# Optimization experiments

Measured on AMD Instinct MI355X. Metric: run time of the kernel, lower is better.

Reference implementation:

```python
import jax, jax.numpy as jnp
import numpy as np
import math

EPS = 1e-6
MAX_NORM = 1.0 - 1e-3


def _clip_to_ball(x):
    # Keep point strictly inside the unit ball (||x|| < 1).
    norm = jnp.maximum(jnp.linalg.norm(x, axis=-1, keepdims=True), EPS)
    factor = jnp.minimum(MAX_NORM / norm, 1.0)
    return x * factor


def setup_inputs() -> dict:
    key = jax.random.key(0)
    k1, k2 = jax.random.split(key)
    B, C, D = 8192, 4096, 512
    euclidean_emb = jax.random.normal(k1, (B, D), dtype=jnp.float32)
    centroids = jax.random.uniform(k2, (C, D), dtype=jnp.float32, minval=-0.01, maxval=0.01)
    log_c = jnp.asarray(math.log(1.0), dtype=jnp.float32)
    return {"euclidean_emb": euclidean_emb, "log_c": log_c, "centroids": centroids}


def reference(euclidean_emb, log_c, centroids):
    # torch code used c = self.log_c.exp().item() -> c is detached scalar
    c = jax.lax.stop_gradient(jnp.exp(log_c))
    sqrt_c = jnp.sqrt(c)

    # expmap0: Euclidean -> Poincare ball
    v_norm = jnp.maximum(jnp.linalg.norm(euclidean_emb, axis=-1, keepdims=True), EPS)
    coeff = jnp.tanh(sqrt_c * v_norm) / (sqrt_c * v_norm)
    x_h = _clip_to_ball(coeff * euclidean_emb)   # (B, D)
    cen_h = _clip_to_ball(centroids)             # (C, D)

    # Pairwise Poincare distance via GEMM (same math as the expanded (B,C,D) form):
    # ||x - y||^2 = ||x||^2 + ||y||^2 - 2 <x, y>
    x2_raw = jnp.sum(x_h * x_h, axis=-1)         # (B,)
    y2_raw = jnp.sum(cen_h * cen_h, axis=-1)     # (C,)
    x2 = jnp.minimum(x2_raw, MAX_NORM ** 2)
    y2 = jnp.minimum(y2_raw, MAX_NORM ** 2)
    xy = x_h @ cen_h.T                           # (B, C) GEMM
    diff2 = x2_raw[:, None] + y2_raw[None, :] - 2.0 * xy

    denom = jnp.maximum((1.0 - c * x2)[:, None] * (1.0 - c * y2)[None, :], EPS)
    arg = jnp.maximum(1.0 + c * (2.0 * diff2) / denom, 1.0 + EPS)
    dists = jnp.arccosh(arg) / sqrt_c            # (B, C)
    return dists, x_h, cen_h
```

## Files before the change

### kernel.cpp

```cpp
#include <hip/hip_runtime.h>
#include <math.h>

#define EPSV 1e-6f
#define MAX_NORM (1.0f - 1e-3f)

typedef __attribute__((ext_vector_type(8))) short short8;
typedef __attribute__((ext_vector_type(4))) float f32x4;

__device__ inline ushort f32_to_bf16(float f) {
    union { float f; uint32_t u; } cv;
    cv.f = f;
    uint32_t u = cv.u;
    u += 0x7FFFu + ((u >> 16) & 1u);
    return (ushort)(u >> 16);
}

__device__ inline void glds16(const ushort* gsrc, ushort* ldsdst) {
    auto* g = (const __attribute__((address_space(1))) uint32_t*)gsrc;
    auto* l = (__attribute__((address_space(3))) uint32_t*)ldsdst;
    __builtin_amdgcn_global_load_lds(g, l, 16, 0, 0);
}

__device__ inline short8 ds_read128(const ushort* p) {
    auto* l3 = (const __attribute__((address_space(3))) ushort*)p;
    const uint32_t addr = (uint32_t)(uintptr_t)l3;
    short8 v;
    asm volatile("ds_read_b128 %0, %1" : "=&v"(v) : "v"(addr));
    return v;
}

__global__ void rows_emb_kernel(const float* __restrict__ emb,
                                const float* __restrict__ logc,
                                float* __restrict__ xh,
                                ushort* __restrict__ xbf,
                                float* __restrict__ x2raw,
                                float* __restrict__ dxv) {
    const int D = 512;
    const int row = blockIdx.x;
    const int lane = threadIdx.x;

    const float4* r4 = (const float4*)(emb + (size_t)row * D);
    float4 a = r4[2 * lane];
    float4 b = r4[2 * lane + 1];

    float ss = a.x * a.x + a.y * a.y + a.z * a.z + a.w * a.w
             + b.x * b.x + b.y * b.y + b.z * b.z + b.w * b.w;
#pragma unroll
    for (int off = 32; off > 0; off >>= 1) ss += __shfl_xor(ss, off, 64);

    const float c  = expf(logc[0]);
    const float sc = sqrtf(c);

    const float tn    = sqrtf(ss);
    const float vn    = fmaxf(tn, EPSV);
    const float coeff = tanhf(sc * vn) / (sc * vn);
    const float pre   = coeff * tn;
    const float fac   = fminf(MAX_NORM / fmaxf(pre, EPSV), 1.0f);
    const float scale = coeff * fac;

    float4 oa, ob;
    oa.x = a.x * scale; oa.y = a.y * scale; oa.z = a.z * scale; oa.w = a.w * scale;
    ob.x = b.x * scale; ob.y = b.y * scale; ob.z = b.z * scale; ob.w = b.w * scale;

    float4* o4 = (float4*)(xh + (size_t)row * D);
    o4[2 * lane]     = oa;
    o4[2 * lane + 1] = ob;

    union { ushort u[8]; uint4 v; } pk;
    pk.u[0] = f32_to_bf16(oa.x); pk.u[1] = f32_to_bf16(oa.y);
    pk.u[2] = f32_to_bf16(oa.z); pk.u[3] = f32_to_bf16(oa.w);
    pk.u[4] = f32_to_bf16(ob.x); pk.u[5] = f32_to_bf16(ob.y);
    pk.u[6] = f32_to_bf16(ob.z); pk.u[7] = f32_to_bf16(ob.w);
    ((uint4*)(xbf + (size_t)row * D))[lane] = pk.v;

    if (lane == 0) {
        const float sq = scale * scale * ss;
        x2raw[row] = sq;
        dxv[row]   = 1.0f - c * fminf(sq, MAX_NORM * MAX_NORM);
    }
}

__global__ void rows_cen_kernel(const float* __restrict__ cen,
                                const float* __restrict__ logc,
                                float* __restrict__ ch,
                                ushort* __restrict__ cbf,
                                float* __restrict__ y2raw,
                                float* __restrict__ dyv) {
    const int D = 512;
    const int row = blockIdx.x;
    const int lane = threadIdx.x;

    const float4* r4 = (const float4*)(cen + (size_t)row * D);
    float4 a = r4[2 * lane];
    float4 b = r4[2 * lane + 1];

    float ss = a.x * a.x + a.y * a.y + a.z * a.z + a.w * a.w
             + b.x * b.x + b.y * b.y + b.z * b.z + b.w * b.w;
#pragma unroll
    for (int off = 32; off > 0; off >>= 1) ss += __shfl_xor(ss, off, 64);

    const float c = expf(logc[0]);

    const float tn    = sqrtf(ss);
    const float scale = fminf(MAX_NORM / fmaxf(tn, EPSV), 1.0f);

    float4 oa, ob;
    oa.x = a.x * scale; oa.y = a.y * scale; oa.z = a.z * scale; oa.w = a.w * scale;
    ob.x = b.x * scale; ob.y = b.y * scale; ob.z = b.z * scale; ob.w = b.w * scale;

    float4* o4 = (float4*)(ch + (size_t)row * D);
    o4[2 * lane]     = oa;
    o4[2 * lane + 1] = ob;

    union { ushort u[8]; uint4 v; } pk;
    pk.u[0] = f32_to_bf16(oa.x); pk.u[1] = f32_to_bf16(oa.y);
    pk.u[2] = f32_to_bf16(oa.z); pk.u[3] = f32_to_bf16(oa.w);
    pk.u[4] = f32_to_bf16(ob.x); pk.u[5] = f32_to_bf16(ob.y);
    pk.u[6] = f32_to_bf16(ob.z); pk.u[7] = f32_to_bf16(ob.w);
    ((uint4*)(cbf + (size_t)row * D))[lane] = pk.v;

    if (lane == 0) {
        const float sq = scale * scale * ss;
        y2raw[row] = sq;
        dyv[row]   = 1.0f - c * fminf(sq, MAX_NORM * MAX_NORM);
    }
}

#define BM 256
#define BN 256
#define BKT 32
#define EPST 68

__global__ __launch_bounds__(512, 2)
void gemm_epi_kernel(const ushort* __restrict__ Abf,
                     const ushort* __restrict__ Bbf,
                     const float* __restrict__ x2raw,
                     const float* __restrict__ dxv,
                     const float* __restrict__ y2raw,
                     const float* __restrict__ dyv,
                     const float* __restrict__ logc,
                     float* __restrict__ out,
                     int M, int N, int K) {
    __shared__ __align__(16) char smem[4 * 32768];

    const int tid  = threadIdx.x;
    const int lane = tid & 63;
    const int wid  = tid >> 6;
    const int wm   = wid >> 2;
    const int wn   = wid & 3;

    const int bm = blockIdx.y;
    const int bn = blockIdx.x;

    const ushort* Ab = Abf + (size_t)bm * BM * K;
    const ushort* Bb = Bbf + (size_t)bn * BN * K;

    f32x4 acc[8][4];
#pragma unroll
    for (int m = 0; m < 8; m++)
#pragma unroll
        for (int n = 0; n < 4; n++) acc[m][n] = (f32x4){0.f, 0.f, 0.f, 0.f};

    const size_t fragoff = (size_t)(lane & 15) * K + ((lane >> 4) * 8);

    auto Abuf = [&](int b) { return (ushort*)(smem + b * 32768); };
    auto Bbuf = [&](int b) { return (ushort*)(smem + b * 32768 + 16384); };

    auto stage_call = [&](int b, int k0, int j) {
        const int s = wid * 2 + (j & 1);
        const size_t goff = (size_t)(s * 16) * K + k0 + fragoff;
        if (j < 2) glds16(Ab + goff, Abuf(b) + s * 512);
        else       glds16(Bb + goff, Bbuf(b) + s * 512);
    };

    const int NT = K / BKT;

#pragma unroll
    for (int tt = 0; tt < 3; ++tt)
#pragma unroll
        for (int j = 0; j < 4; ++j)
            stage_call(tt & 3, tt * BKT, j);

    for (int t = 0; t < NT; ++t) {
        const int b = t & 3;

        if (t <= NT - 3)      asm volatile("s_waitcnt vmcnt(8)" ::: "memory");
        else if (t == NT - 2) asm volatile("s_waitcnt vmcnt(4)" ::: "memory");
        else                  asm volatile("s_waitcnt vmcnt(0)" ::: "memory");
        __builtin_amdgcn_s_barrier();

        const bool do_stage = (t + 3 < NT);
        const int  sb = (t + 3) & 3;
        const int  sk = (t + 3) * BKT;

        short8 af[8], bfr[4];
#pragma unroll
        for (int n = 0; n < 4; n++)
            bfr[n] = ds_read128(Bbuf(b) + (wn * 4 + n) * 512 + lane * 8);
        af[0] = ds_read128(Abuf(b) + (wm * 8 + 0) * 512 + lane * 8);
        af[1] = ds_read128(Abuf(b) + (wm * 8 + 1) * 512 + lane * 8);

#pragma unroll
        for (int q = 0; q < 4; ++q) {
            if (do_stage) stage_call(sb, sk, q);
            if (q < 3) {
                af[2 * q + 2] = ds_read128(Abuf(b) + (wm * 8 + 2 * q + 2) * 512 + lane * 8);
                af[2 * q + 3] = ds_read128(Abuf(b) + (wm * 8 + 2 * q + 3) * 512 + lane * 8);
                asm volatile("s_waitcnt lgkmcnt(2)" ::: "memory");
            } else {
                asm volatile("s_waitcnt lgkmcnt(0)" ::: "memory");
            }
            __builtin_amdgcn_sched_barrier(0);
            __builtin_amdgcn_s_setprio(1);
#pragma unroll
            for (int mm = 0; mm < 2; mm++)
#pragma unroll
                for (int n = 0; n < 4; n++)
                    acc[2 * q + mm][n] = __builtin_amdgcn_mfma_f32_16x16x32_bf16(
                        af[2 * q + mm], bfr[n], acc[2 * q + mm][n], 0, 0, 0);
            __builtin_amdgcn_s_setprio(0);
        }
    }

    __syncthreads();

    const float c   = expf(logc[0]);
    const float rsc = 1.0f / sqrtf(c);
    const int l16 = lane & 15;
    const int lg  = lane >> 4;

    float* ep = (float*)(smem + (size_t)wid * 4352);
    const int gr_base = bm * BM + wm * 128;
    const int gc_base = bn * BN + wn * 64;

#pragma unroll
    for (int m = 0; m < 8; m++) {
#pragma unroll
        for (int n = 0; n < 4; n++)
#pragma unroll
            for (int r = 0; r < 4; r++)
                ep[(lg * 4 + r) * EPST + n * 16 + l16] = acc[m][n][r];
        asm volatile("s_waitcnt lgkmcnt(0)" ::: "memory");

#pragma unroll
        for (int it = 0; it < 4; it++) {
            const int row = it * 4 + lg;
            const int gr  = gr_base + m * 16 + row;
            const int gc  = gc_base + l16 * 4;
            float4 xy4 = *(const float4*)&ep[row * EPST + l16 * 4];
            const float rx  = x2raw[gr];
            const float dxr = dxv[gr];
            const float4 ry4 = *(const float4*)&y2raw[gc];
            const float4 dy4 = *(const float4*)&dyv[gc];
            float4 o;
            {
                const float rden = __builtin_amdgcn_rcpf(fmaxf(dxr * dy4.x, EPSV));
                float t = fmaxf(2.0f * c * (rx + ry4.x - 2.0f * xy4.x) * rden, EPSV);
                o.x = __logf(1.0f + t + __builtin_amdgcn_sqrtf(t * (t + 2.0f))) * rsc;
            }
            {
                const float rden = __builtin_amdgcn_rcpf(fmaxf(dxr * dy4.y, EPSV));
                float t = fmaxf(2.0f * c * (rx + ry4.y - 2.0f * xy4.y) * rden, EPSV);
                o.y = __logf(1.0f + t + __builtin_amdgcn_sqrtf(t * (t + 2.0f))) * rsc;
            }
            {
                const float rden = __builtin_amdgcn_rcpf(fmaxf(dxr * dy4.z, EPSV));
                float t = fmaxf(2.0f * c * (rx + ry4.z - 2.0f * xy4.z) * rden, EPSV);
                o.z = __logf(1.0f + t + __builtin_amdgcn_sqrtf(t * (t + 2.0f))) * rsc;
            }
            {
                const float rden = __builtin_amdgcn_rcpf(fmaxf(dxr * dy4.w, EPSV));
                float t = fmaxf(2.0f * c * (rx + ry4.w - 2.0f * xy4.w) * rden, EPSV);
                o.w = __logf(1.0f + t + __builtin_amdgcn_sqrtf(t * (t + 2.0f))) * rsc;
            }
            *(float4*)&out[(size_t)gr * N + gc] = o;
        }
        asm volatile("s_waitcnt lgkmcnt(0)" ::: "memory");
    }
}

extern "C" void kernel_launch(void* const* d_in, const int* in_sizes, int n_in,
                              void* d_out, int out_size, void* d_ws, size_t ws_size,
                              hipStream_t stream) {
    const float* emb  = (const float*)d_in[0];
    const float* logc = (const float*)d_in[1];
    const float* cen  = (const float*)d_in[2];

    const int D = 512;
    const int B = in_sizes[0] / D;
    const int C = in_sizes[2] / D;

    float* out   = (float*)d_out;
    float* dists = out;
    float* xh    = out + (size_t)B * C;
    float* ch    = xh + (size_t)B * D;

    char* ws = (char*)d_ws;
    size_t off = 0;
    auto alloc = [&](size_t bytes) -> char* {
        char* p = ws + off;
        off += (bytes + 255) & ~(size_t)255;
        return p;
    };
    ushort* xbf   = (ushort*)alloc((size_t)B * D * sizeof(ushort));
    ushort* cbf   = (ushort*)alloc((size_t)C * D * sizeof(ushort));
    float*  x2raw = (float*)alloc((size_t)B * sizeof(float));
    float*  dxv   = (float*)alloc((size_t)B * sizeof(float));
    float*  y2raw = (float*)alloc((size_t)C * sizeof(float));
    float*  dyv   = (float*)alloc((size_t)C * sizeof(float));

    rows_emb_kernel<<<B, 64, 0, stream>>>(emb, logc, xh, xbf, x2raw, dxv);
    rows_cen_kernel<<<C, 64, 0, stream>>>(cen, logc, ch, cbf, y2raw, dyv);

    dim3 grid(C / BN, B / BM);
    gemm_epi_kernel<<<grid, 512, 0, stream>>>(xbf, cbf, x2raw, dxv, y2raw, dyv,
                                              logc, dists, B, C, D);
}
```

Before: 86.99 us.

## Double the K tile to 64 and switch to a two-stage LDS ring

Raises the GEMM K step from 32 to 64 and replaces the four-buffer, three-ahead prefetch ring with a two-buffer double-buffered pipeline. Each iteration now issues twice as many MFMAs per barrier, and the problem dimensions (K, number of iterations, output stride) are hardcoded as compile-time constants. The aim is to cut barrier and loop overhead. In exchange, prefetch depth drops to one tile, and every iteration waits on vmcnt(0), which may expose global-load latency. LDS use stays at 128KB.

```diff
diff --git a/kernel.cpp b/kernel.cpp
--- a/kernel.cpp
+++ b/kernel.cpp
@@ -128,8 +128,11 @@
 
 #define BM 256
 #define BN 256
-#define BKT 32
+#define BKT 64
 #define EPST 68
+#define KDIM 512
+#define NT 8
+#define NCOLS 4096
 
 __global__ __launch_bounds__(512, 2)
 void gemm_epi_kernel(const ushort* __restrict__ Abf,
@@ -139,9 +142,8 @@
                      const float* __restrict__ y2raw,
                      const float* __restrict__ dyv,
                      const float* __restrict__ logc,
-                     float* __restrict__ out,
-                     int M, int N, int K) {
-    __shared__ __align__(16) char smem[4 * 32768];
+                     float* __restrict__ out) {
+    __shared__ __align__(16) ushort ring[2][32768];
 
     const int tid  = threadIdx.x;
     const int lane = tid & 63;
@@ -152,8 +154,8 @@
     const int bm = blockIdx.y;
     const int bn = blockIdx.x;
 
-    const ushort* Ab = Abf + (size_t)bm * BM * K;
-    const ushort* Bb = Bbf + (size_t)bn * BN * K;
+    const ushort* Ab = Abf + (size_t)bm * BM * KDIM;
+    const ushort* Bb = Bbf + (size_t)bn * BN * KDIM;
 
     f32x4 acc[8][4];
 #pragma unroll
@@ -161,63 +163,80 @@
 #pragma unroll
         for (int n = 0; n < 4; n++) acc[m][n] = (f32x4){0.f, 0.f, 0.f, 0.f};
 
-    const size_t fragoff = (size_t)(lane & 15) * K + ((lane >> 4) * 8);
-
-    auto Abuf = [&](int b) { return (ushort*)(smem + b * 32768); };
-    auto Bbuf = [&](int b) { return (ushort*)(smem + b * 32768 + 16384); };
-
-    auto stage_call = [&](int b, int k0, int j) {
-        const int s = wid * 2 + (j & 1);
-        const size_t goff = (size_t)(s * 16) * K + k0 + fragoff;
-        if (j < 2) glds16(Ab + goff, Abuf(b) + s * 512);
-        else       glds16(Bb + goff, Bbuf(b) + s * 512);
-    };
-
-    const int NT = K / BKT;
-
-#pragma unroll
-    for (int tt = 0; tt < 3; ++tt)
-#pragma unroll
-        for (int j = 0; j < 4; ++j)
-            stage_call(tt & 3, tt * BKT, j);
+    const size_t fragoff = (size_t)(lane & 15) * KDIM + ((lane >> 4) * 8);
+
+    const ushort* gA0 = Ab + (size_t)(2 * wid * 16) * KDIM + fragoff;
+    const ushort* gA1 = gA0 + 16 * KDIM;
+    const ushort* gB0 = Bb + (size_t)(2 * wid * 16) * KDIM + fragoff;
+    const ushort* gB1 = gB0 + 16 * KDIM;
+
+    ushort* lA = &ring[0][0]     + wid * 2048;
+    ushort* lB = &ring[0][16384] + wid * 2048;
+
+    const ushort* rdA = &ring[0][0]     + wm * 8192 + lane * 8;
+    const ushort* rdB = &ring[0][16384] + wn * 4096 + lane * 8;
+
+    glds16(gA0,      lA);        glds16(gA0 + 32, lA + 512);
+    glds16(gA1,      lA + 1024); glds16(gA1 + 32, lA + 1536);
+    glds16(gB0,      lB);        glds16(gB0 + 32, lB + 512);
+    glds16(gB1,      lB + 1024); glds16(gB1 + 32, lB + 1536);
 
     for (int t = 0; t < NT; ++t) {
-        const int b = t & 3;
-
-        if (t <= NT - 3)      asm volatile("s_waitcnt vmcnt(8)" ::: "memory");
-        else if (t == NT - 2) asm volatile("s_waitcnt vmcnt(4)" ::: "memory");
-        else                  asm volatile("s_waitcnt vmcnt(0)" ::: "memory");
+        asm volatile("s_waitcnt vmcnt(0)" ::: "memory");
         __builtin_amdgcn_s_barrier();
-
-        const bool do_stage = (t + 3 < NT);
-        const int  sb = (t + 3) & 3;
-        const int  sk = (t + 3) * BKT;
-
-        short8 af[8], bfr[4];
-#pragma unroll
-        for (int n = 0; n < 4; n++)
-            bfr[n] = ds_read128(Bbuf(b) + (wn * 4 + n) * 512 + lane * 8);
-        af[0] = ds_read128(Abuf(b) + (wm * 8 + 0) * 512 + lane * 8);
-        af[1] = ds_read128(Abuf(b) + (wm * 8 + 1) * 512 + lane * 8);
+        __builtin_amdgcn_sched_barrier(0);
+
+        const int p32 = (t & 1) * 32768;
+        const ushort* rA = rdA + p32;
+        const ushort* rB = rdB + p32;
+
+        const bool st = (t + 1 < NT);
+        const int koff = (t + 1) * BKT;
+        const int spd  = ((t + 1) & 1) * 32768;
+        const ushort* sA0 = gA0 + koff;
+        const ushort* sA1 = gA1 + koff;
+        const ushort* sB0 = gB0 + koff;
+        const ushort* sB1 = gB1 + koff;
+
+        short8 bf[8], af[16];
+#pragma unroll
+        for (int n = 0; n < 4; n++) {
+            bf[2 * n]     = ds_read128(rB + n * 1024);
+            bf[2 * n + 1] = ds_read128(rB + n * 1024 + 512);
+        }
+        af[0] = ds_read128(rA);
+        af[1] = ds_read128(rA + 512);
+        af[2] = ds_read128(rA + 1024);
+        af[3] = ds_read128(rA + 1536);
 
 #pragma unroll
         for (int q = 0; q < 4; ++q) {
-            if (do_stage) stage_call(sb, sk, q);
+            if (st) {
+                if (q == 0) { glds16(sA0, lA + spd);        glds16(sA0 + 32, lA + spd + 512); }
+                if (q == 1) { glds16(sA1, lA + spd + 1024); glds16(sA1 + 32, lA + spd + 1536); }
+                if (q == 2) { glds16(sB0, lB + spd);        glds16(sB0 + 32, lB + spd + 512); }
+                if (q == 3) { glds16(sB1, lB + spd + 1024); glds16(sB1 + 32, lB + spd + 1536); }
+            }
             if (q < 3) {
-                af[2 * q + 2] = ds_read128(Abuf(b) + (wm * 8 + 2 * q + 2) * 512 + lane * 8);
-                af[2 * q + 3] = ds_read128(Abuf(b) + (wm * 8 + 2 * q + 3) * 512 + lane * 8);
-                asm volatile("s_waitcnt lgkmcnt(2)" ::: "memory");
+                af[4 * q + 4] = ds_read128(rA + (2 * q + 2) * 1024);
+                af[4 * q + 5] = ds_read128(rA + (2 * q + 2) * 1024 + 512);
+                af[4 * q + 6] = ds_read128(rA + (2 * q + 3) * 1024);
+                af[4 * q + 7] = ds_read128(rA + (2 * q + 3) * 1024 + 512);
+                asm volatile("s_waitcnt lgkmcnt(4)" ::: "memory");
             } else {
                 asm volatile("s_waitcnt lgkmcnt(0)" ::: "memory");
             }
             __builtin_amdgcn_sched_barrier(0);
             __builtin_amdgcn_s_setprio(1);
 #pragma unroll
-            for (int mm = 0; mm < 2; mm++)
-#pragma unroll
-                for (int n = 0; n < 4; n++)
-                    acc[2 * q + mm][n] = __builtin_amdgcn_mfma_f32_16x16x32_bf16(
-                        af[2 * q + mm], bfr[n], acc[2 * q + mm][n], 0, 0, 0);
+            for (int kk = 0; kk < 2; kk++)
+#pragma unroll
+                for (int n = 0; n < 4; n++) {
+                    acc[2 * q][n] = __builtin_amdgcn_mfma_f32_16x16x32_bf16(
+                        af[4 * q + kk], bf[2 * n + kk], acc[2 * q][n], 0, 0, 0);
+                    acc[2 * q + 1][n] = __builtin_amdgcn_mfma_f32_16x16x32_bf16(
+                        af[4 * q + 2 + kk], bf[2 * n + kk], acc[2 * q + 1][n], 0, 0, 0);
+                }
             __builtin_amdgcn_s_setprio(0);
         }
     }
@@ -229,7 +248,7 @@
     const int l16 = lane & 15;
     const int lg  = lane >> 4;
 
-    float* ep = (float*)(smem + (size_t)wid * 4352);
+    float* ep = (float*)((char*)&ring[0][0] + (size_t)wid * 4352);
     const int gr_base = bm * BM + wm * 128;
     const int gc_base = bn * BN + wn * 64;
 
@@ -273,7 +292,7 @@
                 float t = fmaxf(2.0f * c * (rx + ry4.w - 2.0f * xy4.w) * rden, EPSV);
                 o.w = __logf(1.0f + t + __builtin_amdgcn_sqrtf(t * (t + 2.0f))) * rsc;
             }
-            *(float4*)&out[(size_t)gr * N + gc] = o;
+            *(float4*)&out[(size_t)gr * NCOLS + gc] = o;
         }
         asm volatile("s_waitcnt lgkmcnt(0)" ::: "memory");
     }
@@ -314,5 +333,5 @@
 
     dim3 grid(C / BN, B / BM);
     gemm_epi_kernel<<<grid, 512, 0, stream>>>(xbf, cbf, x2raw, dxv, y2raw, dyv,
-                                              logc, dists, B, C, D);
-}
+                                              logc, dists);
+}
```

After: 91.75 us. 5.5% more time.
